# Optimization experiments

Measured on AMD Instinct MI355X. Metric: run time of the kernel, lower is better.

## Reference

```python
import jax, jax.numpy as jnp
import numpy as np

V, E, H = 50000, 300, 512            # vocab, embed dim, rnn hidden
BS, NSEG, SLEN = 64, 3, 256          # batch, segments per sample (hardcoded 3), max seg len
NNODE, NFEAT, NHID, NOUT = 18, 600, 600, 1024  # GCN dims (hardcoded in module)


def _uniform(k, shape, stdv):
    return jax.random.uniform(k, shape, jnp.float32, -stdv, stdv)


def setup_inputs() -> dict:
    key = jax.random.key(0)
    ks = jax.random.split(key, 14)
    input_inds = jax.random.randint(ks[0], (BS, NSEG, SLEN), 0, V, dtype=jnp.int32)
    input_lens = jax.random.randint(ks[1], (BS, NSEG), 1, SLEN + 1, dtype=jnp.int32)
    emb = jax.random.normal(ks[2], (V, E), jnp.float32) * 0.1
    # GRU params (torch layout: [3H, in])
    sx = float(np.sqrt(6.0 / (3 * H + E)))
    sh = float(np.sqrt(6.0 / (3 * H + H)))
    w_ih = _uniform(ks[3], (3 * H, E), sx)
    w_hh = _uniform(ks[4], (3 * H, H), sh)
    b_ih = jnp.zeros((3 * H,), jnp.float32)
    b_hh = jnp.zeros((3 * H,), jnp.float32)
    # GCN params (uniform +-1/sqrt(out_features), per reset_parameters)
    s1 = 1.0 / float(np.sqrt(NHID))
    s2 = 1.0 / float(np.sqrt(NOUT))
    gw1 = _uniform(ks[5], (NFEAT, NHID), s1)
    gb1 = _uniform(ks[6], (NHID,), s1)
    gw2 = _uniform(ks[7], (NHID, NOUT), s2)
    gb2 = _uniform(ks[8], (NOUT,), s2)
    sg_x = jax.random.normal(ks[9], (BS, NNODE, NFEAT), jnp.float32)
    adj = jax.random.uniform(ks[10], (BS, NNODE, NNODE), jnp.float32)
    return dict(input_inds=input_inds, input_lens=input_lens, emb=emb,
                w_ih=w_ih, w_hh=w_hh, b_ih=b_ih, b_hh=b_hh,
                sg_x=sg_x, adj=adj, gw1=gw1, gb1=gb1, gw2=gw2, gb2=gb2)


def _gru(x, lens, w_ih, w_hh, b_ih, b_hh):
    """Length-masked batched GRU. x: [B,T,E], lens: [B]. Returns ys [B,T,H], hT [B,H]
    where hT equals the hidden state at the last valid step (carry frozen after len)."""
    B, T, _ = x.shape
    Hh = w_hh.shape[1]
    xi = jnp.einsum('bte,ge->btg', x, w_ih) + b_ih  # precompute input gates [B,T,3H]

    def step(h, inp):
        xi_t, t = inp
        gh = h @ w_hh.T + b_hh
        xr, xz, xn = jnp.split(xi_t, 3, axis=-1)
        hr, hz, hn = jnp.split(gh, 3, axis=-1)
        r = jax.nn.sigmoid(xr + hr)
        z = jax.nn.sigmoid(xz + hz)
        n = jnp.tanh(xn + r * hn)
        h_new = (1.0 - z) * n + z * h
        h_out = jnp.where((t < lens)[:, None], h_new, h)
        return h_out, h_out

    h0 = jnp.zeros((B, Hh), x.dtype)
    hT, ys = jax.lax.scan(step, h0, (jnp.swapaxes(xi, 0, 1), jnp.arange(T)))
    return jnp.swapaxes(ys, 0, 1), hT


def reference(input_inds, input_lens, emb, w_ih, w_hh, b_ih, b_hh,
              sg_x, adj, gw1, gb1, gw2, gb2):
    B3 = BS * NSEG
    T = NSEG * SLEN
    tok = emb[input_inds.reshape(B3, SLEN)]           # [B3, SLEN, E]
    ys, hT = _gru(tok, input_lens.reshape(B3), w_ih, w_hh, b_ih, b_hh)

    # Pack valid (segment, t) outputs contiguously per sample (the torch cat of
    # per-segment ragged outputs), pad tail with zeros.
    lens = input_lens                                            # [BS, NSEG]
    offs = jnp.concatenate([jnp.zeros((BS, 1), jnp.int32),
                            jnp.cumsum(lens, axis=1)[:, :-1]], axis=1)
    t_idx = jnp.arange(SLEN, dtype=jnp.int32)
    valid = t_idx[None, None, :] < lens[:, :, None]              # [BS, NSEG, SLEN]
    pos = jnp.where(valid, offs[:, :, None] + t_idx[None, None, :], T)
    pos = pos.reshape(BS, T)
    b_ix = jnp.arange(BS)[:, None]
    out_rfts = jnp.zeros((BS, T + 1, H), ys.dtype).at[b_ix, pos].set(
        ys.reshape(BS, T, H))[:, :T]
    out_embs = jnp.zeros((BS, T + 1, E), tok.dtype).at[b_ix, pos].set(
        tok.reshape(BS, T, E))[:, :T]
    tlen = jnp.sum(lens, axis=1)
    out_msks = (jnp.arange(T)[None, :] < tlen[:, None]).astype(jnp.float32)
    out_hids = hT.reshape(BS, NSEG, H)                           # final h per segment

    # GCN: relu(adj @ (x W1) + b1); adj @ (h W2) + b2
    h1 = jax.nn.relu(jnp.einsum('bnm,bmf->bnf', adj, sg_x @ gw1) + gb1)
    out_sg = jnp.einsum('bnm,bmf->bnf', adj, h1 @ gw2) + gb2
    return out_rfts, out_embs, out_msks, out_sg, out_hids
```

## Files before the change

### kernel.cpp

```cpp
#include <hip/hip_runtime.h>


typedef unsigned short ushort_t;
typedef __attribute__((ext_vector_type(8))) short bf16x8;
typedef __attribute__((ext_vector_type(4))) float f32x4;

#define OUT_RFTS 0UL
#define OUT_EMBS 25165824UL
#define OUT_MSKS 39911424UL
#define OUT_SG   39960576UL
#define OUT_HIDS 41140224UL

#define WS_HX   0UL
#define WS_FLG  393216UL
#define WS_H1   405504UL

__device__ __forceinline__ ushort_t f2b(float f) {
  unsigned int u = __float_as_uint(f);
  u += 0x7fffu + ((u >> 16) & 1u);
  return (ushort_t)(u >> 16);
}

union FRAG { ushort_t s[8]; bf16x8 v; uint2 u2[2]; };

__device__ __forceinline__ bf16x8 frag_from_f32(const float* p, bool v0, bool v1) {
  float4 a = v0 ? *(const float4*)p       : make_float4(0.f, 0.f, 0.f, 0.f);
  float4 b = v1 ? *(const float4*)(p + 4) : make_float4(0.f, 0.f, 0.f, 0.f);
  FRAG u;
  u.s[0] = f2b(a.x); u.s[1] = f2b(a.y); u.s[2] = f2b(a.z); u.s[3] = f2b(a.w);
  u.s[4] = f2b(b.x); u.s[5] = f2b(b.y); u.s[6] = f2b(b.z); u.s[7] = f2b(b.w);
  return u.v;
}

__global__ __launch_bounds__(256, 1) void gru_fused(
    const int* __restrict__ inds, const int* __restrict__ lens,
    const float* __restrict__ emb, const float* __restrict__ w_ih,
    const float* __restrict__ w_hh, const float* __restrict__ b_ih,
    const float* __restrict__ b_hh, ushort_t* __restrict__ hx,
    unsigned int* __restrict__ flags, float* __restrict__ out)
{
  const int g = blockIdx.x >> 3;
  const int p = blockIdx.x & 7;
  const int tid = threadIdx.x;
  const int w = tid >> 6;
  const int l = tid & 63;
  const int jc = l & 15;
  const int quad = l >> 4;
  const int jg = p * 64 + w * 16 + jc;

  __shared__ ushort_t hst[16 * 520];
  __shared__ ushort_t tokb[2][16 * 328];
  __shared__ int sidx[16];

  bf16x8 bwh[3][16];
#pragma unroll
  for (int g3 = 0; g3 < 3; ++g3) {
    const float* wr = w_hh + (size_t)(g3 * 512 + jg) * 512 + quad * 8;
#pragma unroll
    for (int kc = 0; kc < 16; ++kc)
      bwh[g3][kc] = frag_from_f32(wr + kc * 32, true, true);
  }
  bf16x8 bwx[3][10];
#pragma unroll
  for (int g3 = 0; g3 < 3; ++g3) {
    const float* wr = w_ih + (size_t)(g3 * 512 + jg) * 300;
#pragma unroll
    for (int kc = 0; kc < 10; ++kc) {
      const int k0 = kc * 32 + quad * 8;
      bwx[g3][kc] = frag_from_f32(wr + k0, k0 + 3 < 300, k0 + 7 < 300);
    }
  }
  const float bsr = b_ih[jg] + b_hh[jg];
  const float bsz = b_ih[512 + jg] + b_hh[512 + jg];
  const float bin = b_ih[1024 + jg];
  const float bhn = b_hh[1024 + jg];

  int Tg = 0;
  for (int i = 0; i < 16; ++i) Tg = max(Tg, lens[g * 16 + i]);

  int len_q[4]; size_t rf_q[4], hxo_q[4], hid_q[4];
  float h_q[4] = {0.f, 0.f, 0.f, 0.f};
#pragma unroll
  for (int q = 0; q < 4; ++q) {
    int sl = quad * 4 + q;
    int b3 = g * 16 + sl;
    len_q[q] = lens[b3];
    int b = b3 / 3, seg = b3 - b * 3;
    int off = 0;
    for (int ss = 0; ss < seg; ++ss) off += lens[b * 3 + ss];
    rf_q[q]  = OUT_RFTS + ((size_t)b * 768 + off) * 512 + jg;
    hxo_q[q] = (size_t)b3 * 512 + (size_t)(jg & ~1);
    hid_q[q] = OUT_HIDS + (size_t)b3 * 512 + jg;
  }

  int trow[5], tcu[5];
#pragma unroll
  for (int c = 0; c < 5; ++c) {
    int u = c * 256 + tid;
    trow[c] = u / 80;
    tcu[c]  = u - trow[c] * 80;
  }

  if (tid < 16) sidx[tid] = inds[(size_t)(g * 16 + tid) * 256 + 0];
  __syncthreads();
#pragma unroll
  for (int c = 0; c < 5; ++c) {
    float4 v = make_float4(0.f, 0.f, 0.f, 0.f);
    if (tcu[c] < 75)
      v = *(const float4*)(emb + (size_t)sidx[trow[c]] * 300 + tcu[c] * 4);
    FRAG u; u.s[0] = f2b(v.x); u.s[1] = f2b(v.y); u.s[2] = f2b(v.z); u.s[3] = f2b(v.w);
    *(uint2*)(&tokb[0][trow[c] * 328 + tcu[c] * 4]) = u.u2[0];
  }
  __syncthreads();

  const int HXE = 192 * 512;
  const f32x4 z4 = {0.f, 0.f, 0.f, 0.f};

  for (int t = 0; t < Tg; ++t) {
    const int buf = t & 1, nbuf = buf ^ 1;
    if (tid < 8) {
      long guard = 0;
      while (__hip_atomic_load(&flags[(g * 8 + tid) * 32],
                               __ATOMIC_ACQUIRE, __HIP_MEMORY_SCOPE_AGENT)
             < (unsigned int)t) {
        __builtin_amdgcn_s_sleep(1);
        if (++guard > 20000000L) break;
      }
    }
    if (tid < 16) {
      int tt = (t + 1 < 256) ? t + 1 : 255;
      sidx[tid] = inds[(size_t)(g * 16 + tid) * 256 + tt];
    }
    __syncthreads();
    {
      const unsigned long long* src =
          (const unsigned long long*)(hx + (size_t)buf * HXE + (size_t)g * 16 * 512);
#pragma unroll
      for (int c = 0; c < 8; ++c) {
        int idx = c * 256 + tid;
        unsigned long long v = __hip_atomic_load(
            (unsigned long long*)(src + idx), __ATOMIC_RELAXED, __HIP_MEMORY_SCOPE_AGENT);
        int row = idx >> 7, col = idx & 127;
        *(unsigned long long*)(&hst[row * 520 + col * 4]) = v;
      }
    }
    __syncthreads();
    float4 tr[5];
#pragma unroll
    for (int c = 0; c < 5; ++c) {
      tr[c] = make_float4(0.f, 0.f, 0.f, 0.f);
      if (tcu[c] < 75)
        tr[c] = *(const float4*)(emb + (size_t)sidx[trow[c]] * 300 + tcu[c] * 4);
    }
    f32x4 accr = z4, accz = z4, anh = z4, anx = z4;
#pragma unroll
    for (int kc = 0; kc < 16; ++kc) {
      bf16x8 af = *(const bf16x8*)(&hst[(l & 15) * 520 + kc * 32 + quad * 8]);
      accr = __builtin_amdgcn_mfma_f32_16x16x32_bf16(af, bwh[0][kc], accr, 0, 0, 0);
      accz = __builtin_amdgcn_mfma_f32_16x16x32_bf16(af, bwh[1][kc], accz, 0, 0, 0);
      anh  = __builtin_amdgcn_mfma_f32_16x16x32_bf16(af, bwh[2][kc], anh, 0, 0, 0);
    }
#pragma unroll
    for (int kc = 0; kc < 10; ++kc) {
      bf16x8 xf = *(const bf16x8*)(&tokb[buf][(l & 15) * 328 + kc * 32 + quad * 8]);
      accr = __builtin_amdgcn_mfma_f32_16x16x32_bf16(xf, bwx[0][kc], accr, 0, 0, 0);
      accz = __builtin_amdgcn_mfma_f32_16x16x32_bf16(xf, bwx[1][kc], accz, 0, 0, 0);
      anx  = __builtin_amdgcn_mfma_f32_16x16x32_bf16(xf, bwx[2][kc], anx, 0, 0, 0);
    }
    ushort_t* hxout = hx + (size_t)nbuf * HXE;
#pragma unroll
    for (int q = 0; q < 4; ++q) {
      float pr = accr[q] + bsr;
      float pz = accz[q] + bsz;
      float r = 1.f / (1.f + __expf(-pr));
      float z = 1.f / (1.f + __expf(-pz));
      float e2 = __expf(2.f * (anx[q] + bin + r * (anh[q] + bhn)));
      float n = 1.f - 2.f / (e2 + 1.f);
      float hn = (1.f - z) * n + z * h_q[q];
      bool valid = (t < len_q[q]);
      hn = valid ? hn : h_q[q];
      h_q[q] = hn;
      if (valid) out[rf_q[q] + (size_t)t * 512] = hn;
      unsigned int hb = f2b(hn);
      unsigned int ob = (unsigned int)__shfl_xor((int)hb, 1, 64) & 0xffffu;
      if ((jc & 1) == 0) {
        unsigned int pv = (hb & 0xffffu) | (ob << 16);
        __hip_atomic_store((unsigned int*)(hxout + hxo_q[q]), pv,
                           __ATOMIC_RELAXED, __HIP_MEMORY_SCOPE_AGENT);
      }
    }
#pragma unroll
    for (int c = 0; c < 5; ++c) {
      FRAG u;
      u.s[0] = f2b(tr[c].x); u.s[1] = f2b(tr[c].y);
      u.s[2] = f2b(tr[c].z); u.s[3] = f2b(tr[c].w);
      *(uint2*)(&tokb[nbuf][trow[c] * 328 + tcu[c] * 4]) = u.u2[0];
    }
    __syncthreads();
    if (tid == 0)
      __hip_atomic_store(&flags[(g * 8 + p) * 32], (unsigned int)(t + 1),
                         __ATOMIC_RELEASE, __HIP_MEMORY_SCOPE_AGENT);
  }
#pragma unroll
  for (int q = 0; q < 4; ++q) out[hid_q[q]] = h_q[q];
}

__global__ __launch_bounds__(256, 4) void pack_embs(
    const int* __restrict__ inds, const int* __restrict__ lens,
    const float* __restrict__ emb, float* __restrict__ out)
{
  const int b = blockIdx.y;
  const int p = blockIdx.x * 4 + (threadIdx.x >> 6);
  const int l = threadIdx.x & 63;
  const int l0 = lens[b * 3], l1 = lens[b * 3 + 1], l2 = lens[b * 3 + 2];
  const int tlen = l0 + l1 + l2;
  if (l == 0)
    out[OUT_MSKS + (size_t)b * 768 + p] = (p < tlen) ? 1.0f : 0.0f;
  const size_t rfoff = OUT_RFTS + ((size_t)b * 768 + p) * 512;
  const size_t eboff = OUT_EMBS + ((size_t)b * 768 + p) * 300;
  if (p >= tlen) {
    const float4 z4 = make_float4(0.f, 0.f, 0.f, 0.f);
    *(float4*)(out + rfoff + (size_t)l * 8)     = z4;
    *(float4*)(out + rfoff + (size_t)l * 8 + 4) = z4;
    for (int u = l; u < 75; u += 64)
      *(float4*)(out + eboff + (size_t)u * 4) = z4;
  } else {
    int s, tt;
    if (p < l0)           { s = 0; tt = p; }
    else if (p < l0 + l1) { s = 1; tt = p - l0; }
    else                  { s = 2; tt = p - l0 - l1; }
    const int ind = inds[(b * 3 + s) * 256 + tt];
    const float* src = emb + (size_t)ind * 300;
    for (int u = l; u < 75; u += 64)
      *(float4*)(out + eboff + (size_t)u * 4) = *(const float4*)(src + (size_t)u * 4);
  }
}

__global__ __launch_bounds__(256, 2) void gcn1(
    const float* __restrict__ sgx, const float* __restrict__ adj,
    const float* __restrict__ gw1, const float* __restrict__ gb1,
    float* __restrict__ h1)
{
  const int cb = blockIdx.x, b = blockIdx.y;
  const int tid = threadIdx.x;
  __shared__ float xs[18 * 600];
  __shared__ float adjs[324];
  __shared__ float ts[1152];
  for (int i = tid; i < 18 * 600; i += 256) xs[i] = sgx[(size_t)b * 10800 + i];
  for (int i = tid; i < 324; i += 256) adjs[i] = adj[(size_t)b * 324 + i];
  __syncthreads();
  const int c0 = cb * 64;
  for (int o = tid; o < 1152; o += 256) {
    const int r = o >> 6, c = c0 + (o & 63);
    float a0 = 0.f, a1 = 0.f;
    if (c < 600) {
      const float* xr = xs + r * 600;
      for (int k = 0; k < 600; k += 2) {
        a0 += xr[k]     * gw1[(size_t)k * 600 + c];
        a1 += xr[k + 1] * gw1[(size_t)(k + 1) * 600 + c];
      }
    }
    ts[o] = a0 + a1;
  }
  __syncthreads();
  for (int o = tid; o < 1152; o += 256) {
    const int n = o >> 6, cl = o & 63, c = c0 + cl;
    if (c >= 600) continue;
    float acc = gb1[c];
#pragma unroll
    for (int m = 0; m < 18; ++m) acc += adjs[n * 18 + m] * ts[m * 64 + cl];
    h1[(size_t)b * 10800 + n * 600 + c] = fmaxf(acc, 0.f);
  }
}

__global__ __launch_bounds__(256, 2) void gcn2(
    const float* __restrict__ h1, const float* __restrict__ adj,
    const float* __restrict__ gw2, const float* __restrict__ gb2,
    float* __restrict__ out)
{
  const int cb = blockIdx.x, b = blockIdx.y;
  const int tid = threadIdx.x;
  __shared__ float xs[18 * 600];
  __shared__ float adjs[324];
  __shared__ float ts[1152];
  for (int i = tid; i < 18 * 600; i += 256) xs[i] = h1[(size_t)b * 10800 + i];
  for (int i = tid; i < 324; i += 256) adjs[i] = adj[(size_t)b * 324 + i];
  __syncthreads();
  const int c0 = cb * 64;
  for (int o = tid; o < 1152; o += 256) {
    const int r = o >> 6, c = c0 + (o & 63);
    const float* xr = xs + r * 600;
    float a0 = 0.f, a1 = 0.f;
    for (int k = 0; k < 600; k += 2) {
      a0 += xr[k]     * gw2[(size_t)k * 1024 + c];
      a1 += xr[k + 1] * gw2[(size_t)(k + 1) * 1024 + c];
    }
    ts[o] = a0 + a1;
  }
  __syncthreads();
  for (int o = tid; o < 1152; o += 256) {
    const int n = o >> 6, cl = o & 63, c = c0 + cl;
    float acc = gb2[c];
#pragma unroll
    for (int m = 0; m < 18; ++m) acc += adjs[n * 18 + m] * ts[m * 64 + cl];
    out[OUT_SG + (size_t)b * 18432 + n * 1024 + c] = acc;
  }
}

extern "C" void kernel_launch(void* const* d_in, const int* in_sizes, int n_in,
                              void* d_out, int out_size, void* d_ws, size_t ws_size,
                              hipStream_t stream)
{
  (void)in_sizes; (void)n_in; (void)out_size; (void)ws_size;
  const int*   inds = (const int*)d_in[0];
  const int*   lens = (const int*)d_in[1];
  const float* emb  = (const float*)d_in[2];
  const float* w_ih = (const float*)d_in[3];
  const float* w_hh = (const float*)d_in[4];
  const float* b_ih = (const float*)d_in[5];
  const float* b_hh = (const float*)d_in[6];
  const float* sgx  = (const float*)d_in[7];
  const float* adj  = (const float*)d_in[8];
  const float* gw1  = (const float*)d_in[9];
  const float* gb1  = (const float*)d_in[10];
  const float* gw2  = (const float*)d_in[11];
  const float* gb2  = (const float*)d_in[12];
  float* out = (float*)d_out;
  char* ws = (char*)d_ws;
  ushort_t* hx = (ushort_t*)(ws + WS_HX);
  unsigned int* flags = (unsigned int*)(ws + WS_FLG);
  float* h1 = (float*)(ws + WS_H1);

  hipMemsetAsync(ws, 0, 405504, stream);
  gru_fused<<<dim3(96),      256, 0, stream>>>(inds, lens, emb, w_ih, w_hh,
                                               b_ih, b_hh, hx, flags, out);
  pack_embs<<<dim3(192, 64), 256, 0, stream>>>(inds, lens, emb, out);
  gcn1     <<<dim3(10, 64),  256, 0, stream>>>(sgx, adj, gw1, gb1, h1);
  gcn2     <<<dim3(16, 64),  256, 0, stream>>>(h1, adj, gw2, gb2, out);
}
```

Baseline: 2.296 ms.

## Fuse GRU, GCN and embedding packing into one concurrent launch

Merges the four kernels into one 256-block kernel. Blocks 0-95 run the recurrent GRU, blocks 96-159 each compute the full two-layer GCN for one sample with h1 kept in shared memory, and the remaining blocks pack embeddings, masks and zero padding. The GCN and packing work now runs alongside the latency-bound GRU instead of after it, and the h1 workspace round trip is gone. The flag spin now uses a relaxed load followed by an explicit agent-scope acquire fence. Costs: every block reserves about 92KB of LDS, and each GCN block does all column tiles serially, so GCN work is far less parallel.

```diff
diff --git a/kernel.cpp b/kernel.cpp
--- a/kernel.cpp
+++ b/kernel.cpp
@@ -13,7 +13,6 @@
 
 #define WS_HX   0UL
 #define WS_FLG  393216UL
-#define WS_H1   405504UL
 
 __device__ __forceinline__ ushort_t f2b(float f) {
   unsigned int u = __float_as_uint(f);
@@ -32,278 +31,277 @@
   return u.v;
 }
 
-__global__ __launch_bounds__(256, 1) void gru_fused(
+__global__ __launch_bounds__(256, 1) void fused_all(
     const int* __restrict__ inds, const int* __restrict__ lens,
     const float* __restrict__ emb, const float* __restrict__ w_ih,
     const float* __restrict__ w_hh, const float* __restrict__ b_ih,
-    const float* __restrict__ b_hh, ushort_t* __restrict__ hx,
-    unsigned int* __restrict__ flags, float* __restrict__ out)
-{
-  const int g = blockIdx.x >> 3;
-  const int p = blockIdx.x & 7;
-  const int tid = threadIdx.x;
-  const int w = tid >> 6;
-  const int l = tid & 63;
-  const int jc = l & 15;
-  const int quad = l >> 4;
-  const int jg = p * 64 + w * 16 + jc;
-
-  __shared__ ushort_t hst[16 * 520];
-  __shared__ ushort_t tokb[2][16 * 328];
-  __shared__ int sidx[16];
-
-  bf16x8 bwh[3][16];
-#pragma unroll
-  for (int g3 = 0; g3 < 3; ++g3) {
-    const float* wr = w_hh + (size_t)(g3 * 512 + jg) * 512 + quad * 8;
-#pragma unroll
-    for (int kc = 0; kc < 16; ++kc)
-      bwh[g3][kc] = frag_from_f32(wr + kc * 32, true, true);
-  }
-  bf16x8 bwx[3][10];
-#pragma unroll
-  for (int g3 = 0; g3 < 3; ++g3) {
-    const float* wr = w_ih + (size_t)(g3 * 512 + jg) * 300;
-#pragma unroll
-    for (int kc = 0; kc < 10; ++kc) {
-      const int k0 = kc * 32 + quad * 8;
-      bwx[g3][kc] = frag_from_f32(wr + k0, k0 + 3 < 300, k0 + 7 < 300);
-    }
-  }
-  const float bsr = b_ih[jg] + b_hh[jg];
-  const float bsz = b_ih[512 + jg] + b_hh[512 + jg];
-  const float bin = b_ih[1024 + jg];
-  const float bhn = b_hh[1024 + jg];
-
-  int Tg = 0;
-  for (int i = 0; i < 16; ++i) Tg = max(Tg, lens[g * 16 + i]);
-
-  int len_q[4]; size_t rf_q[4], hxo_q[4], hid_q[4];
-  float h_q[4] = {0.f, 0.f, 0.f, 0.f};
-#pragma unroll
-  for (int q = 0; q < 4; ++q) {
-    int sl = quad * 4 + q;
-    int b3 = g * 16 + sl;
-    len_q[q] = lens[b3];
-    int b = b3 / 3, seg = b3 - b * 3;
-    int off = 0;
-    for (int ss = 0; ss < seg; ++ss) off += lens[b * 3 + ss];
-    rf_q[q]  = OUT_RFTS + ((size_t)b * 768 + off) * 512 + jg;
-    hxo_q[q] = (size_t)b3 * 512 + (size_t)(jg & ~1);
-    hid_q[q] = OUT_HIDS + (size_t)b3 * 512 + jg;
-  }
-
-  int trow[5], tcu[5];
-#pragma unroll
-  for (int c = 0; c < 5; ++c) {
-    int u = c * 256 + tid;
-    trow[c] = u / 80;
-    tcu[c]  = u - trow[c] * 80;
-  }
-
-  if (tid < 16) sidx[tid] = inds[(size_t)(g * 16 + tid) * 256 + 0];
-  __syncthreads();
-#pragma unroll
-  for (int c = 0; c < 5; ++c) {
-    float4 v = make_float4(0.f, 0.f, 0.f, 0.f);
-    if (tcu[c] < 75)
-      v = *(const float4*)(emb + (size_t)sidx[trow[c]] * 300 + tcu[c] * 4);
-    FRAG u; u.s[0] = f2b(v.x); u.s[1] = f2b(v.y); u.s[2] = f2b(v.z); u.s[3] = f2b(v.w);
-    *(uint2*)(&tokb[0][trow[c] * 328 + tcu[c] * 4]) = u.u2[0];
-  }
-  __syncthreads();
-
-  const int HXE = 192 * 512;
-  const f32x4 z4 = {0.f, 0.f, 0.f, 0.f};
-
-  for (int t = 0; t < Tg; ++t) {
-    const int buf = t & 1, nbuf = buf ^ 1;
-    if (tid < 8) {
-      long guard = 0;
-      while (__hip_atomic_load(&flags[(g * 8 + tid) * 32],
-                               __ATOMIC_ACQUIRE, __HIP_MEMORY_SCOPE_AGENT)
-             < (unsigned int)t) {
-        __builtin_amdgcn_s_sleep(1);
-        if (++guard > 20000000L) break;
-      }
-    }
-    if (tid < 16) {
-      int tt = (t + 1 < 256) ? t + 1 : 255;
-      sidx[tid] = inds[(size_t)(g * 16 + tid) * 256 + tt];
-    }
-    __syncthreads();
-    {
-      const unsigned long long* src =
-          (const unsigned long long*)(hx + (size_t)buf * HXE + (size_t)g * 16 * 512);
-#pragma unroll
-      for (int c = 0; c < 8; ++c) {
-        int idx = c * 256 + tid;
-        unsigned long long v = __hip_atomic_load(
-            (unsigned long long*)(src + idx), __ATOMIC_RELAXED, __HIP_MEMORY_SCOPE_AGENT);
-        int row = idx >> 7, col = idx & 127;
-        *(unsigned long long*)(&hst[row * 520 + col * 4]) = v;
-      }
-    }
-    __syncthreads();
-    float4 tr[5];
-#pragma unroll
-    for (int c = 0; c < 5; ++c) {
-      tr[c] = make_float4(0.f, 0.f, 0.f, 0.f);
-      if (tcu[c] < 75)
-        tr[c] = *(const float4*)(emb + (size_t)sidx[trow[c]] * 300 + tcu[c] * 4);
-    }
-    f32x4 accr = z4, accz = z4, anh = z4, anx = z4;
-#pragma unroll
-    for (int kc = 0; kc < 16; ++kc) {
-      bf16x8 af = *(const bf16x8*)(&hst[(l & 15) * 520 + kc * 32 + quad * 8]);
-      accr = __builtin_amdgcn_mfma_f32_16x16x32_bf16(af, bwh[0][kc], accr, 0, 0, 0);
-      accz = __builtin_amdgcn_mfma_f32_16x16x32_bf16(af, bwh[1][kc], accz, 0, 0, 0);
-      anh  = __builtin_amdgcn_mfma_f32_16x16x32_bf16(af, bwh[2][kc], anh, 0, 0, 0);
-    }
-#pragma unroll
-    for (int kc = 0; kc < 10; ++kc) {
-      bf16x8 xf = *(const bf16x8*)(&tokb[buf][(l & 15) * 328 + kc * 32 + quad * 8]);
-      accr = __builtin_amdgcn_mfma_f32_16x16x32_bf16(xf, bwx[0][kc], accr, 0, 0, 0);
-      accz = __builtin_amdgcn_mfma_f32_16x16x32_bf16(xf, bwx[1][kc], accz, 0, 0, 0);
-      anx  = __builtin_amdgcn_mfma_f32_16x16x32_bf16(xf, bwx[2][kc], anx, 0, 0, 0);
-    }
-    ushort_t* hxout = hx + (size_t)nbuf * HXE;
-#pragma unroll
-    for (int q = 0; q < 4; ++q) {
-      float pr = accr[q] + bsr;
-      float pz = accz[q] + bsz;
-      float r = 1.f / (1.f + __expf(-pr));
-      float z = 1.f / (1.f + __expf(-pz));
-      float e2 = __expf(2.f * (anx[q] + bin + r * (anh[q] + bhn)));
-      float n = 1.f - 2.f / (e2 + 1.f);
-      float hn = (1.f - z) * n + z * h_q[q];
-      bool valid = (t < len_q[q]);
-      hn = valid ? hn : h_q[q];
-      h_q[q] = hn;
-      if (valid) out[rf_q[q] + (size_t)t * 512] = hn;
-      unsigned int hb = f2b(hn);
-      unsigned int ob = (unsigned int)__shfl_xor((int)hb, 1, 64) & 0xffffu;
-      if ((jc & 1) == 0) {
-        unsigned int pv = (hb & 0xffffu) | (ob << 16);
-        __hip_atomic_store((unsigned int*)(hxout + hxo_q[q]), pv,
-                           __ATOMIC_RELAXED, __HIP_MEMORY_SCOPE_AGENT);
-      }
-    }
-#pragma unroll
-    for (int c = 0; c < 5; ++c) {
-      FRAG u;
-      u.s[0] = f2b(tr[c].x); u.s[1] = f2b(tr[c].y);
-      u.s[2] = f2b(tr[c].z); u.s[3] = f2b(tr[c].w);
-      *(uint2*)(&tokb[nbuf][trow[c] * 328 + tcu[c] * 4]) = u.u2[0];
-    }
-    __syncthreads();
-    if (tid == 0)
-      __hip_atomic_store(&flags[(g * 8 + p) * 32], (unsigned int)(t + 1),
-                         __ATOMIC_RELEASE, __HIP_MEMORY_SCOPE_AGENT);
-  }
-#pragma unroll
-  for (int q = 0; q < 4; ++q) out[hid_q[q]] = h_q[q];
-}
-
-__global__ __launch_bounds__(256, 4) void pack_embs(
-    const int* __restrict__ inds, const int* __restrict__ lens,
-    const float* __restrict__ emb, float* __restrict__ out)
-{
-  const int b = blockIdx.y;
-  const int p = blockIdx.x * 4 + (threadIdx.x >> 6);
-  const int l = threadIdx.x & 63;
-  const int l0 = lens[b * 3], l1 = lens[b * 3 + 1], l2 = lens[b * 3 + 2];
-  const int tlen = l0 + l1 + l2;
-  if (l == 0)
-    out[OUT_MSKS + (size_t)b * 768 + p] = (p < tlen) ? 1.0f : 0.0f;
-  const size_t rfoff = OUT_RFTS + ((size_t)b * 768 + p) * 512;
-  const size_t eboff = OUT_EMBS + ((size_t)b * 768 + p) * 300;
-  if (p >= tlen) {
-    const float4 z4 = make_float4(0.f, 0.f, 0.f, 0.f);
-    *(float4*)(out + rfoff + (size_t)l * 8)     = z4;
-    *(float4*)(out + rfoff + (size_t)l * 8 + 4) = z4;
-    for (int u = l; u < 75; u += 64)
-      *(float4*)(out + eboff + (size_t)u * 4) = z4;
-  } else {
-    int s, tt;
-    if (p < l0)           { s = 0; tt = p; }
-    else if (p < l0 + l1) { s = 1; tt = p - l0; }
-    else                  { s = 2; tt = p - l0 - l1; }
-    const int ind = inds[(b * 3 + s) * 256 + tt];
-    const float* src = emb + (size_t)ind * 300;
-    for (int u = l; u < 75; u += 64)
-      *(float4*)(out + eboff + (size_t)u * 4) = *(const float4*)(src + (size_t)u * 4);
-  }
-}
-
-__global__ __launch_bounds__(256, 2) void gcn1(
+    const float* __restrict__ b_hh,
     const float* __restrict__ sgx, const float* __restrict__ adj,
     const float* __restrict__ gw1, const float* __restrict__ gb1,
-    float* __restrict__ h1)
-{
-  const int cb = blockIdx.x, b = blockIdx.y;
-  const int tid = threadIdx.x;
-  __shared__ float xs[18 * 600];
-  __shared__ float adjs[324];
-  __shared__ float ts[1152];
-  for (int i = tid; i < 18 * 600; i += 256) xs[i] = sgx[(size_t)b * 10800 + i];
-  for (int i = tid; i < 324; i += 256) adjs[i] = adj[(size_t)b * 324 + i];
-  __syncthreads();
-  const int c0 = cb * 64;
-  for (int o = tid; o < 1152; o += 256) {
-    const int r = o >> 6, c = c0 + (o & 63);
-    float a0 = 0.f, a1 = 0.f;
-    if (c < 600) {
-      const float* xr = xs + r * 600;
-      for (int k = 0; k < 600; k += 2) {
-        a0 += xr[k]     * gw1[(size_t)k * 600 + c];
-        a1 += xr[k + 1] * gw1[(size_t)(k + 1) * 600 + c];
-      }
-    }
-    ts[o] = a0 + a1;
-  }
-  __syncthreads();
-  for (int o = tid; o < 1152; o += 256) {
-    const int n = o >> 6, cl = o & 63, c = c0 + cl;
-    if (c >= 600) continue;
-    float acc = gb1[c];
-#pragma unroll
-    for (int m = 0; m < 18; ++m) acc += adjs[n * 18 + m] * ts[m * 64 + cl];
-    h1[(size_t)b * 10800 + n * 600 + c] = fmaxf(acc, 0.f);
-  }
-}
-
-__global__ __launch_bounds__(256, 2) void gcn2(
-    const float* __restrict__ h1, const float* __restrict__ adj,
     const float* __restrict__ gw2, const float* __restrict__ gb2,
+    ushort_t* __restrict__ hx, unsigned int* __restrict__ flags,
     float* __restrict__ out)
 {
-  const int cb = blockIdx.x, b = blockIdx.y;
+  __shared__ __attribute__((aligned(16))) char smem[92304];
+  const int bid = blockIdx.x;
   const int tid = threadIdx.x;
-  __shared__ float xs[18 * 600];
-  __shared__ float adjs[324];
-  __shared__ float ts[1152];
-  for (int i = tid; i < 18 * 600; i += 256) xs[i] = h1[(size_t)b * 10800 + i];
-  for (int i = tid; i < 324; i += 256) adjs[i] = adj[(size_t)b * 324 + i];
-  __syncthreads();
-  const int c0 = cb * 64;
-  for (int o = tid; o < 1152; o += 256) {
-    const int r = o >> 6, c = c0 + (o & 63);
-    const float* xr = xs + r * 600;
-    float a0 = 0.f, a1 = 0.f;
-    for (int k = 0; k < 600; k += 2) {
-      a0 += xr[k]     * gw2[(size_t)k * 1024 + c];
-      a1 += xr[k + 1] * gw2[(size_t)(k + 1) * 1024 + c];
-    }
-    ts[o] = a0 + a1;
-  }
-  __syncthreads();
-  for (int o = tid; o < 1152; o += 256) {
-    const int n = o >> 6, cl = o & 63, c = c0 + cl;
-    float acc = gb2[c];
-#pragma unroll
-    for (int m = 0; m < 18; ++m) acc += adjs[n * 18 + m] * ts[m * 64 + cl];
-    out[OUT_SG + (size_t)b * 18432 + n * 1024 + c] = acc;
+
+  if (bid < 96) {
+    ushort_t* hst = (ushort_t*)smem;
+    ushort_t (*tokb)[16 * 328] = (ushort_t (*)[16 * 328])(smem + 16640);
+    int* sidx = (int*)(smem + 37632);
+
+    const int g = bid >> 3;
+    const int p = bid & 7;
+    const int w = tid >> 6;
+    const int l = tid & 63;
+    const int jc = l & 15;
+    const int quad = l >> 4;
+    const int jg = p * 64 + w * 16 + jc;
+
+    bf16x8 bwh[3][16];
+#pragma unroll
+    for (int g3 = 0; g3 < 3; ++g3) {
+      const float* wr = w_hh + (size_t)(g3 * 512 + jg) * 512 + quad * 8;
+#pragma unroll
+      for (int kc = 0; kc < 16; ++kc)
+        bwh[g3][kc] = frag_from_f32(wr + kc * 32, true, true);
+    }
+    bf16x8 bwx[3][10];
+#pragma unroll
+    for (int g3 = 0; g3 < 3; ++g3) {
+      const float* wr = w_ih + (size_t)(g3 * 512 + jg) * 300;
+#pragma unroll
+      for (int kc = 0; kc < 10; ++kc) {
+        const int k0 = kc * 32 + quad * 8;
+        bwx[g3][kc] = frag_from_f32(wr + k0, k0 + 3 < 300, k0 + 7 < 300);
+      }
+    }
+    const float bsr = b_ih[jg] + b_hh[jg];
+    const float bsz = b_ih[512 + jg] + b_hh[512 + jg];
+    const float bin = b_ih[1024 + jg];
+    const float bhn = b_hh[1024 + jg];
+
+    int Tg = 0;
+    for (int i = 0; i < 16; ++i) Tg = max(Tg, lens[g * 16 + i]);
+
+    int len_q[4]; size_t rf_q[4], hxo_q[4], hid_q[4];
+    float h_q[4] = {0.f, 0.f, 0.f, 0.f};
+#pragma unroll
+    for (int q = 0; q < 4; ++q) {
+      int sl = quad * 4 + q;
+      int b3 = g * 16 + sl;
+      len_q[q] = lens[b3];
+      int b = b3 / 3, seg = b3 - b * 3;
+      int off = 0;
+      for (int ss = 0; ss < seg; ++ss) off += lens[b * 3 + ss];
+      rf_q[q]  = OUT_RFTS + ((size_t)b * 768 + off) * 512 + jg;
+      hxo_q[q] = (size_t)b3 * 512 + (size_t)(jg & ~1);
+      hid_q[q] = OUT_HIDS + (size_t)b3 * 512 + jg;
+    }
+
+    int trow[5], tcu[5];
+#pragma unroll
+    for (int c = 0; c < 5; ++c) {
+      int u = c * 256 + tid;
+      trow[c] = u / 80;
+      tcu[c]  = u - trow[c] * 80;
+    }
+
+    if (tid < 16) sidx[tid] = inds[(size_t)(g * 16 + tid) * 256 + 0];
+    __syncthreads();
+#pragma unroll
+    for (int c = 0; c < 5; ++c) {
+      float4 v = make_float4(0.f, 0.f, 0.f, 0.f);
+      if (tcu[c] < 75)
+        v = *(const float4*)(emb + (size_t)sidx[trow[c]] * 300 + tcu[c] * 4);
+      FRAG u; u.s[0] = f2b(v.x); u.s[1] = f2b(v.y); u.s[2] = f2b(v.z); u.s[3] = f2b(v.w);
+      *(uint2*)(&tokb[0][trow[c] * 328 + tcu[c] * 4]) = u.u2[0];
+    }
+    __syncthreads();
+
+    const int HXE = 192 * 512;
+    const f32x4 z4 = {0.f, 0.f, 0.f, 0.f};
+
+    for (int t = 0; t < Tg; ++t) {
+      const int buf = t & 1, nbuf = buf ^ 1;
+      if (tid < 8) {
+        long guard = 0;
+        while (__hip_atomic_load(&flags[(g * 8 + tid) * 32],
+                                 __ATOMIC_RELAXED, __HIP_MEMORY_SCOPE_AGENT)
+               < (unsigned int)t) {
+          __builtin_amdgcn_s_sleep(1);
+          if (++guard > 20000000L) break;
+        }
+      }
+      if (tid < 64) __builtin_amdgcn_fence(__ATOMIC_ACQUIRE, "agent");
+      if (tid < 16) {
+        int tt = (t + 1 < 256) ? t + 1 : 255;
+        sidx[tid] = inds[(size_t)(g * 16 + tid) * 256 + tt];
+      }
+      __syncthreads();
+      {
+        const unsigned long long* src =
+            (const unsigned long long*)(hx + (size_t)buf * HXE + (size_t)g * 16 * 512);
+#pragma unroll
+        for (int c = 0; c < 8; ++c) {
+          int idx = c * 256 + tid;
+          unsigned long long v = __hip_atomic_load(
+              (unsigned long long*)(src + idx), __ATOMIC_RELAXED, __HIP_MEMORY_SCOPE_AGENT);
+          int row = idx >> 7, col = idx & 127;
+          *(unsigned long long*)(&hst[row * 520 + col * 4]) = v;
+        }
+      }
+      __syncthreads();
+      float4 tr[5];
+#pragma unroll
+      for (int c = 0; c < 5; ++c) {
+        tr[c] = make_float4(0.f, 0.f, 0.f, 0.f);
+        if (tcu[c] < 75)
+          tr[c] = *(const float4*)(emb + (size_t)sidx[trow[c]] * 300 + tcu[c] * 4);
+      }
+      f32x4 accr = z4, accz = z4, anh = z4, anx = z4;
+#pragma unroll
+      for (int kc = 0; kc < 16; ++kc) {
+        bf16x8 af = *(const bf16x8*)(&hst[(l & 15) * 520 + kc * 32 + quad * 8]);
+        accr = __builtin_amdgcn_mfma_f32_16x16x32_bf16(af, bwh[0][kc], accr, 0, 0, 0);
+        accz = __builtin_amdgcn_mfma_f32_16x16x32_bf16(af, bwh[1][kc], accz, 0, 0, 0);
+        anh  = __builtin_amdgcn_mfma_f32_16x16x32_bf16(af, bwh[2][kc], anh, 0, 0, 0);
+      }
+#pragma unroll
+      for (int kc = 0; kc < 10; ++kc) {
+        bf16x8 xf = *(const bf16x8*)(&tokb[buf][(l & 15) * 328 + kc * 32 + quad * 8]);
+        accr = __builtin_amdgcn_mfma_f32_16x16x32_bf16(xf, bwx[0][kc], accr, 0, 0, 0);
+        accz = __builtin_amdgcn_mfma_f32_16x16x32_bf16(xf, bwx[1][kc], accz, 0, 0, 0);
+        anx  = __builtin_amdgcn_mfma_f32_16x16x32_bf16(xf, bwx[2][kc], anx, 0, 0, 0);
+      }
+      ushort_t* hxout = hx + (size_t)nbuf * HXE;
+#pragma unroll
+      for (int q = 0; q < 4; ++q) {
+        float pr = accr[q] + bsr;
+        float pz = accz[q] + bsz;
+        float r = 1.f / (1.f + __expf(-pr));
+        float z = 1.f / (1.f + __expf(-pz));
+        float e2 = __expf(2.f * (anx[q] + bin + r * (anh[q] + bhn)));
+        float n = 1.f - 2.f / (e2 + 1.f);
+        float hn = (1.f - z) * n + z * h_q[q];
+        bool valid = (t < len_q[q]);
+        hn = valid ? hn : h_q[q];
+        h_q[q] = hn;
+        if (valid) out[rf_q[q] + (size_t)t * 512] = hn;
+        unsigned int hb = f2b(hn);
+        unsigned int ob = (unsigned int)__shfl_xor((int)hb, 1, 64) & 0xffffu;
+        if ((jc & 1) == 0) {
+          unsigned int pv = (hb & 0xffffu) | (ob << 16);
+          __hip_atomic_store((unsigned int*)(hxout + hxo_q[q]), pv,
+                             __ATOMIC_RELAXED, __HIP_MEMORY_SCOPE_AGENT);
+        }
+      }
+#pragma unroll
+      for (int c = 0; c < 5; ++c) {
+        FRAG u;
+        u.s[0] = f2b(tr[c].x); u.s[1] = f2b(tr[c].y);
+        u.s[2] = f2b(tr[c].z); u.s[3] = f2b(tr[c].w);
+        *(uint2*)(&tokb[nbuf][trow[c] * 328 + tcu[c] * 4]) = u.u2[0];
+      }
+      __syncthreads();
+      if (tid == 0)
+        __hip_atomic_store(&flags[(g * 8 + p) * 32], (unsigned int)(t + 1),
+                           __ATOMIC_RELAXED, __HIP_MEMORY_SCOPE_AGENT);
+    }
+#pragma unroll
+    for (int q = 0; q < 4; ++q) out[hid_q[q]] = h_q[q];
+
+  } else if (bid < 160) {
+    const int b = bid - 96;
+    float* xs   = (float*)smem;
+    float* h1s  = (float*)smem + 10800;
+    float* adjs = (float*)smem + 21600;
+    float* ts   = (float*)smem + 21924;
+
+    for (int i = tid; i < 18 * 600; i += 256) xs[i] = sgx[(size_t)b * 10800 + i];
+    for (int i = tid; i < 324; i += 256) adjs[i] = adj[(size_t)b * 324 + i];
+    __syncthreads();
+
+    for (int cb = 0; cb < 10; ++cb) {
+      const int c0 = cb * 64;
+      for (int o = tid; o < 1152; o += 256) {
+        const int r = o >> 6, c = c0 + (o & 63);
+        float a0 = 0.f, a1 = 0.f;
+        if (c < 600) {
+          const float* xr = xs + r * 600;
+          for (int k = 0; k < 600; k += 2) {
+            a0 += xr[k]     * gw1[(size_t)k * 600 + c];
+            a1 += xr[k + 1] * gw1[(size_t)(k + 1) * 600 + c];
+          }
+        }
+        ts[o] = a0 + a1;
+      }
+      __syncthreads();
+      for (int o = tid; o < 1152; o += 256) {
+        const int n = o >> 6, cl = o & 63, c = c0 + cl;
+        if (c < 600) {
+          float acc = gb1[c];
+#pragma unroll
+          for (int m = 0; m < 18; ++m) acc += adjs[n * 18 + m] * ts[m * 64 + cl];
+          h1s[n * 600 + c] = fmaxf(acc, 0.f);
+        }
+      }
+      __syncthreads();
+    }
+    for (int cb = 0; cb < 16; ++cb) {
+      const int c0 = cb * 64;
+      for (int o = tid; o < 1152; o += 256) {
+        const int r = o >> 6, c = c0 + (o & 63);
+        const float* xr = h1s + r * 600;
+        float a0 = 0.f, a1 = 0.f;
+        for (int k = 0; k < 600; k += 2) {
+          a0 += xr[k]     * gw2[(size_t)k * 1024 + c];
+          a1 += xr[k + 1] * gw2[(size_t)(k + 1) * 1024 + c];
+        }
+        ts[o] = a0 + a1;
+      }
+      __syncthreads();
+      for (int o = tid; o < 1152; o += 256) {
+        const int n = o >> 6, cl = o & 63, c = c0 + cl;
+        float acc = gb2[c];
+#pragma unroll
+        for (int m = 0; m < 18; ++m) acc += adjs[n * 18 + m] * ts[m * 64 + cl];
+        out[OUT_SG + (size_t)b * 18432 + n * 1024 + c] = acc;
+      }
+      __syncthreads();
+    }
+
+  } else {
+    const int wid = (bid - 160) * 4 + (tid >> 6);
+    const int l = tid & 63;
+    for (int j = 0; j < 128; ++j) {
+      const int pr = wid + 384 * j;
+      const int b = pr / 768;
+      const int p = pr - b * 768;
+      const int l0 = lens[b * 3], l1 = lens[b * 3 + 1], l2 = lens[b * 3 + 2];
+      const int tlen = l0 + l1 + l2;
+      if (l == 0)
+        out[OUT_MSKS + (size_t)b * 768 + p] = (p < tlen) ? 1.0f : 0.0f;
+      const size_t rfoff = OUT_RFTS + ((size_t)b * 768 + p) * 512;
+      const size_t eboff = OUT_EMBS + ((size_t)b * 768 + p) * 300;
+      if (p >= tlen) {
+        const float4 z4 = make_float4(0.f, 0.f, 0.f, 0.f);
+        *(float4*)(out + rfoff + (size_t)l * 8)     = z4;
+        *(float4*)(out + rfoff + (size_t)l * 8 + 4) = z4;
+        for (int u = l; u < 75; u += 64)
+          *(float4*)(out + eboff + (size_t)u * 4) = z4;
+      } else {
+        int s, tt;
+        if (p < l0)           { s = 0; tt = p; }
+        else if (p < l0 + l1) { s = 1; tt = p - l0; }
+        else                  { s = 2; tt = p - l0 - l1; }
+        const int ind = inds[(b * 3 + s) * 256 + tt];
+        const float* src = emb + (size_t)ind * 300;
+        for (int u = l; u < 75; u += 64)
+          *(float4*)(out + eboff + (size_t)u * 4) = *(const float4*)(src + (size_t)u * 4);
+      }
+    }
   }
 }
 
@@ -329,12 +327,9 @@
   char* ws = (char*)d_ws;
   ushort_t* hx = (ushort_t*)(ws + WS_HX);
   unsigned int* flags = (unsigned int*)(ws + WS_FLG);
-  float* h1 = (float*)(ws + WS_H1);
 
   hipMemsetAsync(ws, 0, 405504, stream);
-  gru_fused<<<dim3(96),      256, 0, stream>>>(inds, lens, emb, w_ih, w_hh,
-                                               b_ih, b_hh, hx, flags, out);
-  pack_embs<<<dim3(192, 64), 256, 0, stream>>>(inds, lens, emb, out);
-  gcn1     <<<dim3(10, 64),  256, 0, stream>>>(sgx, adj, gw1, gb1, h1);
-  gcn2     <<<dim3(16, 64),  256, 0, stream>>>(h1, adj, gw2, gb2, out);
+  fused_all<<<dim3(256), 256, 0, stream>>>(inds, lens, emb, w_ih, w_hh, b_ih, b_hh,
+                                           sgx, adj, gw1, gb1, gw2, gb2,
+                                           hx, flags, out);
 }
```

Measured after the change: 1.878 ms. 18.2% less time.
